# Optimization experiments

Hardware: AMD Instinct MI355X
Metric: run time of the kernel (lower is better)

The kernel has to match this reference:

```python
import jax, jax.numpy as jnp
import numpy as np

B, L, H, OUT = 128, 256, 512, 256


def setup_inputs() -> dict:
    key = jax.random.key(0)
    ks = jax.random.split(key, 13)
    s = 1.0 / np.sqrt(H)
    u = lambda k, shape: jax.random.uniform(k, shape, jnp.float32, -s, s)
    C = jax.random.normal(ks[0], (L, H), jnp.float32)
    # strictly increasing observation times per sample
    dt0 = jax.random.uniform(ks[1], (B, L, 1), jnp.float32)
    t = jnp.cumsum(dt0, axis=1)
    mask = jax.random.randint(ks[2], (B, L, H), 0, 2).astype(jnp.int32)
    # GRU-D parameters: fused gate weights [z | r | candidate]
    Wx = u(ks[3], (H, 3 * H))   # input -> gates
    Wh = u(ks[4], (H, 3 * H))   # hidden -> gates
    Wm = u(ks[5], (H, 3 * H))   # mask  -> gates
    b = u(ks[6], (3 * H,))
    w_gx = u(ks[7], (H,))       # diagonal input-decay weight
    b_gx = u(ks[8], (H,))
    W_gh = u(ks[9], (H, H))     # hidden-decay weight
    b_gh = u(ks[10], (H,))
    W_out = u(ks[11], (H, OUT))
    b_out = u(ks[12], (OUT,))
    return dict(C=C, t=t, mask=mask, Wx=Wx, Wh=Wh, Wm=Wm, b=b, w_gx=w_gx,
                b_gx=b_gx, W_gh=W_gh, b_gh=b_gh, W_out=W_out, b_out=b_out)


def _grud_decode(C, t, mask_f, Wx, Wh, Wm, b, w_gx, b_gx, W_gh, b_gh, W_out, b_out):
    Bn, Ln = t.shape[0], t.shape[1]
    Hn = C.shape[1]
    m = mask_f                                                     # (B,L,H) float 0/1
    tt = jnp.broadcast_to(t[:, :, 0:1], (Bn, Ln, Hn))              # (B,L,H)
    dt = tt - jnp.concatenate([tt[:, :1], tt[:, :-1]], axis=1)     # dt[:,0]=0
    x = jnp.broadcast_to(C[None], (Bn, Ln, Hn))
    # empirical mean of observed values per sample/feature
    x_mean = jnp.sum(m * x, axis=1) / jnp.maximum(jnp.sum(m, axis=1), 1.0)  # (B,H)

    def step(carry, inp):
        h, x_last, d_prev, m_prev = carry
        xi, mi, dti = inp                                          # xi:(H,), mi/dti:(B,H)
        # time since last observation (GRU-D delta recurrence)
        delta = dti + (1.0 - m_prev) * d_prev
        gamma_x = jnp.exp(-jnp.maximum(0.0, w_gx * delta + b_gx))  # input decay
        gamma_h = jnp.exp(-jnp.maximum(0.0, delta @ W_gh + b_gh))  # hidden decay
        x_hat = mi * xi + (1.0 - mi) * (gamma_x * x_last + (1.0 - gamma_x) * x_mean)
        h = gamma_h * h
        pre = x_hat @ Wx + mi @ Wm + b                             # (B,3H)
        zr = jax.nn.sigmoid(pre[:, :2 * Hn] + h @ Wh[:, :2 * Hn])
        z, r = zr[:, :Hn], zr[:, Hn:]
        h_tilde = jnp.tanh(pre[:, 2 * Hn:] + (r * h) @ Wh[:, 2 * Hn:])
        h_new = (1.0 - z) * h + z * h_tilde
        x_last = mi * xi + (1.0 - mi) * x_last
        return (h_new, x_last, delta, mi), h_new

    init = (jnp.zeros((Bn, Hn), C.dtype), x_mean,
            jnp.zeros((Bn, Hn), C.dtype), jnp.ones((Bn, Hn), C.dtype))
    xs = (C, jnp.transpose(m, (1, 0, 2)), jnp.transpose(dt, (1, 0, 2)))
    _, h_seq = jax.lax.scan(step, init, xs)                        # (L,B,H)
    h_seq = jnp.transpose(h_seq, (1, 0, 2))                        # (B,L,H) == permute(1,0,2)
    return h_seq @ W_out + b_out                                   # (B,L,OUT)


def reference(C, t, mask, Wx, Wh, Wm, b, w_gx, b_gx, W_gh, b_gh, W_out, b_out):
    return _grud_decode(C, t, mask.astype(C.dtype), Wx, Wh, Wm, b,
                        w_gx, b_gx, W_gh, b_gh, W_out, b_out)
```

## Files before the change

### kernel.cpp

```cpp
#include <hip/hip_runtime.h>
#include <hip/hip_bf16.h>
#include <hip/hip_fp16.h>
#include <stdint.h>

typedef short bf16x8 __attribute__((ext_vector_type(8)));
typedef unsigned short u16x8 __attribute__((ext_vector_type(8)));
typedef float f32x4  __attribute__((ext_vector_type(4)));
typedef __hip_bfloat16 bf16;

#define MFMA16(a,b,c) __builtin_amdgcn_mfma_f32_16x16x32_bf16((a),(b),(c),0,0,0)

__device__ __forceinline__ float bf2f(bf16 x){ return __bfloat162float(x); }
__device__ __forceinline__ bf16  f2bf(float x){ return __float2bfloat16(x); }
__device__ __forceinline__ short f2bs(float x){ bf16 t = __float2bfloat16(x); return *(short*)&t; }
__device__ __forceinline__ float bs2f(short s){ bf16 t; *(short*)&t = s; return __bfloat162float(t); }
__device__ __forceinline__ float h2f(unsigned short u){ __half t; *(unsigned short*)&t = u; return __half2float(t); }
__device__ __forceinline__ float sf(float x){ return (fabsf(x) < 1e30f) ? x : 0.f; }

#define NB   128
#define NL   256
#define CH   32
#define MCH  4096
#define NQ   8


__global__ void build_wcatT(const float* __restrict__ Wx, const float* __restrict__ Wm,
                            bf16* __restrict__ dst) {
    int i = blockIdx.x * 256 + threadIdx.x;
    if (i >= 1536 * 1024) return;
    int n = i >> 10, k = i & 1023;
    float v = (k < 512) ? Wx[k * 1536 + n] : Wm[(k - 512) * 1536 + n];
    dst[i] = f2bf(sf(v));
}

__global__ void transpose_f2b(const float* __restrict__ src, bf16* __restrict__ dst,
                              int R, int C) {
    int i = blockIdx.x * 256 + threadIdx.x;
    if (i >= R * C) return;
    int r = i % R, c = i / R;
    dst[i] = f2bf(sf(src[r * C + c]));
}


__global__ void xmean_kernel(const int* __restrict__ mask, const float* __restrict__ Cmat,
                             float* __restrict__ xmean) {
    int g = blockIdx.x * 256 + threadIdx.x;
    int b = g >> 9, h = g & 511;
    float s = 0.f, cnt = 0.f;
    for (int l = 0; l < NL; ++l) {
        int m = mask[(size_t)((b << 8) + l) * 512 + h];
        if (m) { s += sf(Cmat[(l << 9) + h]); cnt += 1.f; }
    }
    xmean[g] = s / fmaxf(cnt, 1.f);
}

__global__ void prep_kernel(const int* __restrict__ mask, const float* __restrict__ Cmat,
                            const float* __restrict__ t_in,
                            const float* __restrict__ w_gx, const float* __restrict__ b_gx,
                            const float* __restrict__ xmean,
                            float* __restrict__ xlastC, float* __restrict__ dprevC,
                            float* __restrict__ mprevC, float* __restrict__ tprevC,
                            bf16* __restrict__ Xcat,
                            bf16* __restrict__ Dbuf,
                            int q) {
    int g = blockIdx.x * 256 + threadIdx.x;
    int b = g >> 9, h = g & 511;
    float wg = sf(w_gx[h]), bg = sf(b_gx[h]);
    float xm = xmean[g];
    float xlast, dprev, mprev, tprev;
    if (q == 0) { xlast = xm; dprev = 0.f; mprev = 1.f; tprev = 0.f; }
    else { xlast = xlastC[g]; dprev = dprevC[g]; mprev = mprevC[g]; tprev = tprevC[g]; }
    for (int ll = 0; ll < CH; ++ll) {
        int l = q * CH + ll;
        float tc = sf(t_in[(b << 8) + l]);
        float dtv = (l == 0) ? 0.f : (tc - tprev);
        tprev = tc;
        float mi = (float)mask[(size_t)((b << 8) + l) * 512 + h];
        float delta = dtv + (1.f - mprev) * dprev;
        float gx = __expf(-fmaxf(wg * delta + bg, 0.f));
        float xi = sf(Cmat[(l << 9) + h]);
        float xh = mi * xi + (1.f - mi) * (gx * xlast + (1.f - gx) * xm);
        size_t row = (size_t)ll * 128 + b;
        Xcat[row * 1024 + h]       = f2bf(xh);
        Xcat[row * 1024 + 512 + h] = f2bf(mi);
        Dbuf[row * 512 + h]        = f2bf(delta);
        xlast = mi * xi + (1.f - mi) * xlast;
        dprev = delta; mprev = mi;
    }
    xlastC[g] = xlast; dprevC[g] = dprev; mprevC[g] = mprev; tprevC[g] = tprev;
}

template <int MODE>
__global__ __launch_bounds__(256) void gemm_bt(const bf16* __restrict__ A,
                                               const bf16* __restrict__ BT,
                                               const float* __restrict__ bias,
                                               void* __restrict__ Cout,
                                               int N, int K, int q) {
    const int nb = N >> 7;
    int bn = blockIdx.x % nb, bm = blockIdx.x / nb;
    __shared__ bf16 As[4096];
    __shared__ bf16 Bs[4096];
    int tid = threadIdx.x, lane = tid & 63, w = tid >> 6;
    int wm = w >> 1, wn = w & 1;
    int quad = lane >> 4, l15 = lane & 15;
    f32x4 acc[4][4];
    #pragma unroll
    for (int i = 0; i < 4; ++i)
        #pragma unroll
        for (int j = 0; j < 4; ++j) acc[i][j] = (f32x4){0.f, 0.f, 0.f, 0.f};

    for (int k0 = 0; k0 < K; k0 += 32) {
        bf16x8 av[2], bv[2];
        #pragma unroll
        for (int cc = 0; cc < 2; ++cc) {
            int c = tid + cc * 256;
            int row = c >> 2, kc = c & 3;
            av[cc] = *(const bf16x8*)(A  + (size_t)(bm * 128 + row) * K + k0 + kc * 8);
            bv[cc] = *(const bf16x8*)(BT + (size_t)(bn * 128 + row) * K + k0 + kc * 8);
        }
        __syncthreads();
        #pragma unroll
        for (int cc = 0; cc < 2; ++cc) {
            int c = tid + cc * 256;
            int row = c >> 2, kc = c & 3;
            *(bf16x8*)&As[(kc * 128 + row) * 8] = av[cc];
            *(bf16x8*)&Bs[(kc * 128 + row) * 8] = bv[cc];
        }
        __syncthreads();
        bf16x8 af[4], bfr[4];
        #pragma unroll
        for (int mt = 0; mt < 4; ++mt)
            af[mt] = *(const bf16x8*)&As[(quad * 128 + wm * 64 + mt * 16 + l15) * 8];
        #pragma unroll
        for (int nt = 0; nt < 4; ++nt)
            bfr[nt] = *(const bf16x8*)&Bs[(quad * 128 + wn * 64 + nt * 16 + l15) * 8];
        #pragma unroll
        for (int mt = 0; mt < 4; ++mt)
            #pragma unroll
            for (int nt = 0; nt < 4; ++nt)
                acc[mt][nt] = MFMA16(af[mt], bfr[nt], acc[mt][nt]);
    }
    int row0 = bm * 128 + wm * 64, col0 = bn * 128 + wn * 64;
    #pragma unroll
    for (int mt = 0; mt < 4; ++mt) {
        #pragma unroll
        for (int nt = 0; nt < 4; ++nt) {
            int col = col0 + nt * 16 + l15;
            float bvf = sf(bias[col]);
            #pragma unroll
            for (int r = 0; r < 4; ++r) {
                int row = row0 + mt * 16 + quad * 4 + r;
                float v = acc[mt][nt][r] + bvf;
                if (MODE == 1)
                    ((__half*)Cout)[(size_t)row * N + col] = __float2half(__expf(-fmaxf(v, 0.f)));
                else if (MODE == 2) {
                    int bb = row & 127, lloc = row >> 7;
                    ((float*)Cout)[(size_t)((bb << 8) + q * CH + lloc) * N + col] = v;
                } else
                    ((bf16*)Cout)[(size_t)row * N + col] = f2bf(v);
            }
        }
    }
}

__global__ __launch_bounds__(512, 1) void scan_kernel(
        const bf16* __restrict__ pre,
        const __half* __restrict__ gammaf,
        const bf16* __restrict__ WhT,
        bf16* __restrict__ hseq,
        float* __restrict__ hcarry,
        bf16* __restrict__ rbuf,
        bf16* __restrict__ hnbuf,
        unsigned* __restrict__ ctr) {
    int bx = blockIdx.x;
    int c = bx & 7, w = bx >> 3;
    int tid = threadIdx.x, lane = tid & 63, v = tid >> 6;
    int wi = (w << 3) | v;
    int quad = lane >> 4, l15 = lane & 15;
    __shared__ bf16 hb[16 * 520];
    __shared__ bf16 rh[16 * 520];

    bf16x8 whz[16], whr[16], whh[16];
    int col0 = wi * 16;
    #pragma unroll
    for (int kf = 0; kf < 16; ++kf) {
        int n = col0 + l15;
        whz[kf] = *(const bf16x8*)(WhT + (size_t)n * 512 + kf * 32 + quad * 8);
        whr[kf] = *(const bf16x8*)(WhT + (size_t)(512 + n) * 512 + kf * 32 + quad * 8);
        whh[kf] = *(const bf16x8*)(WhT + (size_t)(1024 + n) * 512 + kf * 32 + quad * 8);
    }

    bf16* rclu = rbuf  + (size_t)c * 16 * 512;
    bf16* hclu = hnbuf + (size_t)c * 16 * 512;
    const unsigned short* gus = (const unsigned short*)gammaf;
    unsigned* fA = ctr + c * 64;
    unsigned* fB = ctr + c * 64 + 32;

    for (int i = tid; i < 16 * 512; i += 512) {
        int row = i >> 9, col = i & 511;
        int brow = c * 16 + row;
        float g0 = __half2float(gammaf[(size_t)brow * 512 + col]);
        hb[row * 520 + col] = f2bf(hcarry[(size_t)brow * 512 + col] * g0);
    }
    float hfo[4];
    #pragma unroll
    for (int r = 0; r < 4; ++r) {
        int brow = c * 16 + quad * 4 + r;
        int cc = col0 + l15;
        float g0 = __half2float(gammaf[(size_t)brow * 512 + cc]);
        hfo[r] = hcarry[(size_t)brow * 512 + cc] * g0;
    }
    __syncthreads();

    int prow = tid >> 5;
    int pcol = (tid & 31) << 4;

    for (int t = 0; t < CH; ++t) {
        unsigned ep = (unsigned)(t + 1);
        bool lastt = (t == CH - 1);
        float pz[4], prr[4], ph[4], gow[4];
        #pragma unroll
        for (int r = 0; r < 4; ++r) {
            int brow = c * 16 + quad * 4 + r;
            size_t pb = ((size_t)t * 128 + brow) * 1536;
            int cc = col0 + l15;
            pz[r]  = bf2f(pre[pb + cc]);
            prr[r] = bf2f(pre[pb + 512 + cc]);
            ph[r]  = bf2f(pre[pb + 1024 + cc]);
            gow[r] = lastt ? 1.f
                   : __half2float(gammaf[((size_t)(t + 1) * 128 + brow) * 512 + cc]);
        }
        u16x8 gt[2];
        {
            size_t gb = ((size_t)(lastt ? t : t + 1) * 128 + c * 16 + prow) * 512 + pcol;
            #pragma unroll
            for (int j = 0; j < 2; ++j) gt[j] = *(const u16x8*)(gus + gb + j * 8);
        }
        f32x4 az = (f32x4){0.f,0.f,0.f,0.f}, ar = az;
        #pragma unroll
        for (int kf = 0; kf < 16; ++kf) {
            bf16x8 a = *(const bf16x8*)&hb[l15 * 520 + kf * 32 + quad * 8];
            az = MFMA16(a, whz[kf], az);
            ar = MFMA16(a, whr[kf], ar);
        }
        float zv[4];
        #pragma unroll
        for (int r = 0; r < 4; ++r) {
            zv[r] = 1.f / (1.f + __expf(-(az[r] + pz[r])));
            float rv = 1.f / (1.f + __expf(-(ar[r] + prr[r])));
            rclu[(quad * 4 + r) * 512 + col0 + l15] = f2bf(rv);
        }
        __syncthreads();
        if (tid == 0) {
            __hip_atomic_store(&fA[w], ep, __ATOMIC_RELEASE, __HIP_MEMORY_SCOPE_AGENT);
            int guard = 0;
            for (;;) {
                bool ok = true;
                #pragma unroll
                for (int j = 0; j < 4; ++j)
                    ok &= (__hip_atomic_load(&fA[j], __ATOMIC_RELAXED,
                                             __HIP_MEMORY_SCOPE_AGENT) >= ep);
                if (ok || ++guard >= (1 << 17)) break;
                __builtin_amdgcn_s_sleep(1);
            }
            (void)__hip_atomic_load(&fA[0], __ATOMIC_ACQUIRE, __HIP_MEMORY_SCOPE_AGENT);
        }
        __syncthreads();
        #pragma unroll
        for (int j = 0; j < 2; ++j) {
            bf16x8 r8 = *(const bf16x8*)&rclu[prow * 512 + pcol + j * 8];
            bf16x8 h8 = *(const bf16x8*)&hb[prow * 520 + pcol + j * 8];
            bf16x8 o;
            #pragma unroll
            for (int e = 0; e < 8; ++e) o[e] = f2bs(bs2f(r8[e]) * bs2f(h8[e]));
            *(bf16x8*)&rh[prow * 520 + pcol + j * 8] = o;
        }
        __syncthreads();
        f32x4 ah = (f32x4){0.f,0.f,0.f,0.f};
        #pragma unroll
        for (int kf = 0; kf < 16; ++kf) {
            bf16x8 a = *(const bf16x8*)&rh[l15 * 520 + kf * 32 + quad * 8];
            ah = MFMA16(a, whh[kf], ah);
        }
        #pragma unroll
        for (int r = 0; r < 4; ++r) {
            int row = quad * 4 + r;
            int brow = c * 16 + row;
            int cc = col0 + l15;
            float x = ah[r] + ph[r];
            float e = __expf(-2.f * fabsf(x));
            float th = copysignf((1.f - e) / (1.f + e), x);
            float hn = (1.f - zv[r]) * hfo[r] + zv[r] * th;
            bf16 hnb = f2bf(hn);
            hclu[row * 512 + cc] = hnb;
            __builtin_nontemporal_store(*(short*)&hnb,
                (short*)&hseq[((size_t)t * 128 + brow) * 512 + cc]);
            if (lastt)
                __builtin_nontemporal_store(hn, &hcarry[(size_t)brow * 512 + cc]);
            hfo[r] = hn * gow[r];
        }
        __syncthreads();
        if (tid == 0) {
            __hip_atomic_store(&fB[w], ep, __ATOMIC_RELEASE, __HIP_MEMORY_SCOPE_AGENT);
            int guard = 0;
            for (;;) {
                bool ok = true;
                #pragma unroll
                for (int j = 0; j < 4; ++j)
                    ok &= (__hip_atomic_load(&fB[j], __ATOMIC_RELAXED,
                                             __HIP_MEMORY_SCOPE_AGENT) >= ep);
                if (ok || ++guard >= (1 << 17)) break;
                __builtin_amdgcn_s_sleep(1);
            }
            (void)__hip_atomic_load(&fB[0], __ATOMIC_ACQUIRE, __HIP_MEMORY_SCOPE_AGENT);
        }
        __syncthreads();
        #pragma unroll
        for (int j = 0; j < 2; ++j) {
            bf16x8 h8 = *(const bf16x8*)&hclu[prow * 512 + pcol + j * 8];
            bf16x8 o;
            #pragma unroll
            for (int e = 0; e < 8; ++e) {
                float g = lastt ? 1.f : h2f(gt[j][e]);
                o[e] = f2bs(bs2f(h8[e]) * g);
            }
            *(bf16x8*)&hb[prow * 520 + pcol + j * 8] = o;
        }
        __syncthreads();
    }
}


extern "C" void kernel_launch(void* const* d_in, const int* in_sizes, int n_in,
                              void* d_out, int out_size, void* d_ws, size_t ws_size,
                              hipStream_t stream) {
    const float* C     = (const float*)d_in[0];
    const float* t_in  = (const float*)d_in[1];
    const int*   mask  = (const int*)d_in[2];
    const float* Wx    = (const float*)d_in[3];
    const float* Wh    = (const float*)d_in[4];
    const float* Wm    = (const float*)d_in[5];
    const float* bvec  = (const float*)d_in[6];
    const float* w_gx  = (const float*)d_in[7];
    const float* b_gx  = (const float*)d_in[8];
    const float* W_gh  = (const float*)d_in[9];
    const float* b_gh  = (const float*)d_in[10];
    const float* W_out = (const float*)d_in[11];
    const float* b_out = (const float*)d_in[12];

    char* w = (char*)d_ws;
    unsigned* ctr   = (unsigned*)(w + 0);
    float* hcarry   = (float*)(w + 16384);
    float* xmean    = (float*)(w + 278528);
    float* xlastC   = (float*)(w + 540672);
    float* dprevC   = (float*)(w + 802816);
    float* mprevC   = (float*)(w + 1064960);
    float* tprevC   = (float*)(w + 1327104);
    bf16*  wcatT    = (bf16*)(w + 1589248);
    bf16*  wghT     = (bf16*)(w + 4734976);
    bf16*  whT      = (bf16*)(w + 5259264);
    bf16*  woutT    = (bf16*)(w + 6832128);
    bf16*  Xcat     = (bf16*)(w + 7094272);
    bf16*  Dbuf     = (bf16*)(w + 15482880);
    bf16*  pre      = (bf16*)(w + 19677184);
    __half* gamma   = (__half*)(w + 32260096);
    bf16*  hseq     = (bf16*)(w + 36454400);
    bf16*  rbuf     = (bf16*)(w + 40648704);
    bf16*  hnbuf    = (bf16*)(w + 40779776);

    hipMemsetAsync(w, 0, 278528, stream);

    build_wcatT<<<6144, 256, 0, stream>>>(Wx, Wm, wcatT);
    transpose_f2b<<<1024, 256, 0, stream>>>(W_gh, wghT, 512, 512);
    transpose_f2b<<<3072, 256, 0, stream>>>(Wh, whT, 512, 1536);
    transpose_f2b<<<512, 256, 0, stream>>>(W_out, woutT, 512, 256);
    xmean_kernel<<<256, 256, 0, stream>>>(mask, C, xmean);

    for (int q = 0; q < NQ; ++q) {
        prep_kernel<<<256, 256, 0, stream>>>(mask, C, t_in, w_gx, b_gx, xmean,
                                             xlastC, dprevC, mprevC, tprevC,
                                             Xcat, Dbuf, q);
        gemm_bt<0><<<32 * 12, 256, 0, stream>>>(Xcat, wcatT, bvec, (void*)pre, 1536, 1024, q);
        gemm_bt<1><<<32 * 4, 256, 0, stream>>>(Dbuf, wghT, b_gh, (void*)gamma, 512, 512, q);
        scan_kernel<<<32, 512, 0, stream>>>(pre, gamma, whT, hseq, hcarry,
                                            rbuf, hnbuf, ctr + q * 512);
        gemm_bt<2><<<32 * 2, 256, 0, stream>>>(hseq, woutT, b_out, d_out, 256, 512, q);
    }
}
```

Baseline: 3.438 ms.

## Exchange r*h and h across blocks via relaxed 64-bit atomics, drop acquire/release fences

```diff
diff --git a/kernel.cpp b/kernel.cpp
--- a/kernel.cpp
+++ b/kernel.cpp
@@ -7,6 +7,7 @@
 typedef unsigned short u16x8 __attribute__((ext_vector_type(8)));
 typedef float f32x4  __attribute__((ext_vector_type(4)));
 typedef __hip_bfloat16 bf16;
+typedef unsigned long long u64;
 
 #define MFMA16(a,b,c) __builtin_amdgcn_mfma_f32_16x16x32_bf16((a),(b),(c),0,0,0)
 
@@ -169,8 +170,8 @@
         const bf16* __restrict__ WhT,
         bf16* __restrict__ hseq,
         float* __restrict__ hcarry,
-        bf16* __restrict__ rbuf,
-        bf16* __restrict__ hnbuf,
+        u64* __restrict__ rbuf,
+        u64* __restrict__ hnbuf,
         unsigned* __restrict__ ctr) {
     int bx = blockIdx.x;
     int c = bx & 7, w = bx >> 3;
@@ -190,8 +191,8 @@
         whh[kf] = *(const bf16x8*)(WhT + (size_t)(1024 + n) * 512 + kf * 32 + quad * 8);
     }
 
-    bf16* rclu = rbuf  + (size_t)c * 16 * 512;
-    bf16* hclu = hnbuf + (size_t)c * 16 * 512;
+    u64* rclu = rbuf  + (size_t)c * 2048;
+    u64* hclu = hnbuf + (size_t)c * 2048;
     const unsigned short* gus = (const unsigned short*)gammaf;
     unsigned* fA = ctr + c * 64;
     unsigned* fB = ctr + c * 64 + 32;
@@ -212,8 +213,8 @@
     }
     __syncthreads();
 
-    int prow = tid >> 5;
-    int pcol = (tid & 31) << 4;
+    int rrow = tid >> 5, rword = tid & 31;
+    int prow = tid >> 5, pc16 = tid & 31, pcol = pc16 << 4, pregion = pc16 >> 3;
 
     for (int t = 0; t < CH; ++t) {
         unsigned ep = (unsigned)(t + 1);
@@ -248,11 +249,17 @@
         for (int r = 0; r < 4; ++r) {
             zv[r] = 1.f / (1.f + __expf(-(az[r] + pz[r])));
             float rv = 1.f / (1.f + __expf(-(ar[r] + prr[r])));
-            rclu[(quad * 4 + r) * 512 + col0 + l15] = f2bf(rv);
+            rh[(quad * 4 + r) * 520 + col0 + l15] = f2bf(rv * hfo[r]);
+        }
+        __syncthreads();
+        {
+            u64 wv = *(const u64*)&rh[rrow * 520 + w * 128 + rword * 4];
+            __hip_atomic_store(&rclu[rrow * 128 + w * 32 + rword], wv,
+                               __ATOMIC_RELAXED, __HIP_MEMORY_SCOPE_AGENT);
         }
         __syncthreads();
         if (tid == 0) {
-            __hip_atomic_store(&fA[w], ep, __ATOMIC_RELEASE, __HIP_MEMORY_SCOPE_AGENT);
+            __hip_atomic_store(&fA[w], ep, __ATOMIC_RELAXED, __HIP_MEMORY_SCOPE_AGENT);
             int guard = 0;
             for (;;) {
                 bool ok = true;
@@ -260,20 +267,18 @@
                 for (int j = 0; j < 4; ++j)
                     ok &= (__hip_atomic_load(&fA[j], __ATOMIC_RELAXED,
                                              __HIP_MEMORY_SCOPE_AGENT) >= ep);
-                if (ok || ++guard >= (1 << 17)) break;
+                if (ok || ++guard >= (1 << 16)) break;
                 __builtin_amdgcn_s_sleep(1);
             }
-            (void)__hip_atomic_load(&fA[0], __ATOMIC_ACQUIRE, __HIP_MEMORY_SCOPE_AGENT);
-        }
-        __syncthreads();
-        #pragma unroll
-        for (int j = 0; j < 2; ++j) {
-            bf16x8 r8 = *(const bf16x8*)&rclu[prow * 512 + pcol + j * 8];
-            bf16x8 h8 = *(const bf16x8*)&hb[prow * 520 + pcol + j * 8];
-            bf16x8 o;
-            #pragma unroll
-            for (int e = 0; e < 8; ++e) o[e] = f2bs(bs2f(r8[e]) * bs2f(h8[e]));
-            *(bf16x8*)&rh[prow * 520 + pcol + j * 8] = o;
+        }
+        __syncthreads();
+        if (pregion != w) {
+            #pragma unroll
+            for (int j = 0; j < 4; ++j) {
+                u64 wv = __hip_atomic_load(&rclu[prow * 128 + pc16 * 4 + j],
+                                           __ATOMIC_RELAXED, __HIP_MEMORY_SCOPE_AGENT);
+                *(u64*)&rh[prow * 520 + pcol + j * 4] = wv;
+            }
         }
         __syncthreads();
         f32x4 ah = (f32x4){0.f,0.f,0.f,0.f};
@@ -285,23 +290,27 @@
         #pragma unroll
         for (int r = 0; r < 4; ++r) {
             int row = quad * 4 + r;
-            int brow = c * 16 + row;
             int cc = col0 + l15;
             float x = ah[r] + ph[r];
             float e = __expf(-2.f * fabsf(x));
             float th = copysignf((1.f - e) / (1.f + e), x);
             float hn = (1.f - zv[r]) * hfo[r] + zv[r] * th;
-            bf16 hnb = f2bf(hn);
-            hclu[row * 512 + cc] = hnb;
-            __builtin_nontemporal_store(*(short*)&hnb,
-                (short*)&hseq[((size_t)t * 128 + brow) * 512 + cc]);
-            if (lastt)
+            hb[row * 520 + cc] = f2bf(hn);
+            if (lastt) {
+                int brow = c * 16 + row;
                 __builtin_nontemporal_store(hn, &hcarry[(size_t)brow * 512 + cc]);
+            }
             hfo[r] = hn * gow[r];
         }
         __syncthreads();
+        {
+            u64 wv = *(const u64*)&hb[rrow * 520 + w * 128 + rword * 4];
+            __hip_atomic_store(&hclu[rrow * 128 + w * 32 + rword], wv,
+                               __ATOMIC_RELAXED, __HIP_MEMORY_SCOPE_AGENT);
+        }
+        __syncthreads();
         if (tid == 0) {
-            __hip_atomic_store(&fB[w], ep, __ATOMIC_RELEASE, __HIP_MEMORY_SCOPE_AGENT);
+            __hip_atomic_store(&fB[w], ep, __ATOMIC_RELAXED, __HIP_MEMORY_SCOPE_AGENT);
             int guard = 0;
             for (;;) {
                 bool ok = true;
@@ -309,22 +318,41 @@
                 for (int j = 0; j < 4; ++j)
                     ok &= (__hip_atomic_load(&fB[j], __ATOMIC_RELAXED,
                                              __HIP_MEMORY_SCOPE_AGENT) >= ep);
-                if (ok || ++guard >= (1 << 17)) break;
+                if (ok || ++guard >= (1 << 16)) break;
                 __builtin_amdgcn_s_sleep(1);
             }
-            (void)__hip_atomic_load(&fB[0], __ATOMIC_ACQUIRE, __HIP_MEMORY_SCOPE_AGENT);
-        }
-        __syncthreads();
-        #pragma unroll
-        for (int j = 0; j < 2; ++j) {
-            bf16x8 h8 = *(const bf16x8*)&hclu[prow * 512 + pcol + j * 8];
-            bf16x8 o;
-            #pragma unroll
-            for (int e = 0; e < 8; ++e) {
-                float g = lastt ? 1.f : h2f(gt[j][e]);
-                o[e] = f2bs(bs2f(h8[e]) * g);
-            }
-            *(bf16x8*)&hb[prow * 520 + pcol + j * 8] = o;
+        }
+        __syncthreads();
+        u64 hw[4];
+        if (pregion != w) {
+            #pragma unroll
+            for (int j = 0; j < 4; ++j)
+                hw[j] = __hip_atomic_load(&hclu[prow * 128 + pc16 * 4 + j],
+                                          __ATOMIC_RELAXED, __HIP_MEMORY_SCOPE_AGENT);
+        } else {
+            #pragma unroll
+            for (int j = 0; j < 4; ++j)
+                hw[j] = *(const u64*)&hb[prow * 520 + pcol + j * 4];
+        }
+        if (w == 0) {
+            int brow = c * 16 + prow;
+            u64* hs = (u64*)&hseq[((size_t)t * 128 + brow) * 512 + pcol];
+            #pragma unroll
+            for (int j = 0; j < 4; ++j) __builtin_nontemporal_store(hw[j], &hs[j]);
+        }
+        #pragma unroll
+        for (int j = 0; j < 4; ++j) {
+            u16x8* gp = (u16x8*)&gt[0];
+            short o4[4];
+            #pragma unroll
+            for (int e = 0; e < 4; ++e) {
+                short hv = (short)((hw[j] >> (16 * e)) & 0xFFFF);
+                float g = lastt ? 1.f : h2f(((unsigned short*)gp)[j * 4 + e]);
+                o4[e] = f2bs(bs2f(hv) * g);
+            }
+            u64 ov = ((u64)(unsigned short)o4[0]) | ((u64)(unsigned short)o4[1] << 16)
+                   | ((u64)(unsigned short)o4[2] << 32) | ((u64)(unsigned short)o4[3] << 48);
+            *(u64*)&hb[prow * 520 + pcol + j * 4] = ov;
         }
         __syncthreads();
     }
@@ -365,8 +393,8 @@
     bf16*  pre      = (bf16*)(w + 19677184);
     __half* gamma   = (__half*)(w + 32260096);
     bf16*  hseq     = (bf16*)(w + 36454400);
-    bf16*  rbuf     = (bf16*)(w + 40648704);
-    bf16*  hnbuf    = (bf16*)(w + 40779776);
+    u64*   rbuf     = (u64*)(w + 40648704);
+    u64*   hnbuf    = (u64*)(w + 40779776);
 
     hipMemsetAsync(w, 0, 278528, stream);
 
```

Result: faster. 2.864 ms (-16.7%).
